# Kernel tuning notes

Measured on AMD Instinct MI355X. Metric: run time of the kernel, lower is better.

## Reference

```python
import jax, jax.numpy as jnp
import numpy as np

LATENT = 1024

def setup_inputs() -> dict:
    key = jax.random.key(0)
    k1, k2, k3, k4 = jax.random.split(key, 4)
    B, T, D = 64, 512, LATENT
    h_t = jax.random.normal(k1, (B, D), dtype=jnp.float32)
    z = jax.random.normal(k2, (B, T, D), dtype=jnp.float32)
    # nn.Linear(2D, D): weight [D, 2D], bias [D]
    bound = 1.0 / np.sqrt(2 * D)
    W = jax.random.uniform(k3, (D, 2 * D), minval=-bound, maxval=bound, dtype=jnp.float32)
    b = jax.random.uniform(k4, (D,), minval=-bound, maxval=bound, dtype=jnp.float32)
    alpha = jnp.full((D,), 0.1, dtype=jnp.float32)
    return {"h_t": h_t, "z": z, "W": W, "b": b, "alpha": alpha}

def reference(h_t, z, W, b, alpha):
    # Split gate weight into h-part and z-part (concat([h,z]) @ W.T == h@Wh.T + z@Wz.T)
    D = h_t.shape[-1]
    Wh = W[:, :D]  # [D, D]
    Wz = W[:, D:]  # [D, D]
    leak = 1.0 - alpha  # [D]

    def step(h, z_t):
        gate = jax.nn.sigmoid(h @ Wh.T + z_t @ Wz.T + b)
        h_new = jnp.tanh(h * leak + gate * z_t)
        return h_new, h_new

    # scan over time: z is [B, T, D] -> [T, B, D]
    _, hs = jax.lax.scan(step, h_t, jnp.swapaxes(z, 0, 1))
    return jnp.swapaxes(hs, 0, 1)  # [B, T, D]
```

## Files before the change

### kernel.cpp

```cpp
#include <hip/hip_runtime.h>
#include <math.h>


#define D_ 1024
#define B_ 64
#define T_ 512

typedef _Float16 f16;
typedef _Float16 f16x8 __attribute__((ext_vector_type(8)));
typedef _Float16 f16x4 __attribute__((ext_vector_type(4)));
typedef float f32x4 __attribute__((ext_vector_type(4)));
typedef unsigned long long u64;

#define WS_WH16  0L
#define WS_WZ16  2097152L
#define WS_SLOTS 4194304L

__device__ __forceinline__ void gload_lds16(const void* g, void* l) {
  __builtin_amdgcn_global_load_lds(
      (const __attribute__((address_space(1))) void*)(g),
      (__attribute__((address_space(3))) void*)(l), 16, 0, 0);
}

__global__ __launch_bounds__(256) void k_prep(
    const float* __restrict__ W, const float* __restrict__ h0,
    f16* __restrict__ wh16, f16* __restrict__ wz16, u64* __restrict__ slots) {
  const int tid = blockIdx.x * 256 + threadIdx.x;
  {
    const long e = (long)tid * 4;
    const long j = e >> 11, c = e & 2047;
    float4 v = *(const float4*)(W + e);
    f16x4 o = {(f16)v.x, (f16)v.y, (f16)v.z, (f16)v.w};
    f16* dst = (c < D_) ? (wh16 + j * D_ + c) : (wz16 + j * D_ + (c - D_));
    *(f16x4*)dst = o;
  }
  if (tid < 65536) {
    if (tid < 32768) {
      const int b = tid >> 9, p = tid & 511;
      f16 fa = (f16)h0[(long)b * D_ + 2 * p];
      f16 fb = (f16)h0[(long)b * D_ + 2 * p + 1];
      unsigned u = (unsigned)*(unsigned short*)&fa |
                   ((unsigned)*(unsigned short*)&fb << 16);
      slots[tid] = (u64)u;
    } else {
      slots[tid] = 0xFFFFFFFF00000000ull;
    }
  }
}

__global__ __launch_bounds__(256) void k_gemm_zw(
    const float* __restrict__ zf, const f16* __restrict__ wz16,
    const float* __restrict__ bias, float* __restrict__ out) {
  __shared__ f16 ldsA[8 * 512];
  __shared__ f16 ldsB[8 * 512];
  const int tid = threadIdx.x, lane = tid & 63, w = tid >> 6;
  const int r16 = lane & 15, g8 = lane >> 4;
  const int nt = blockIdx.x & 7, mt = blockIdx.x >> 3;
  const long m0 = (long)mt * 128, n0 = (long)nt * 128;
  const int arow = tid >> 1, kh = (tid & 1) * 16;
  const float* gA = zf + (m0 + arow) * D_ + kh;
  const f16* gB = wz16 + (n0 + r16) * D_ + g8 * 8;
  const int wr = w >> 1, wc = w & 1;
  f32x4 acc[4][4] = {};
  float4 ra[4];
#pragma unroll
  for (int q = 0; q < 4; ++q) ra[q] = *(const float4*)(gA + q * 4);

  for (int ks = 0; ks < 32; ++ks) {
    if (ks) __syncthreads();
#pragma unroll
    for (int c = 0; c < 2; ++c) {
      const int ch = w * 2 + c;
      gload_lds16(gB + (long)ch * 16 * D_ + ks * 32, &ldsB[ch * 512]);
    }
    {
      const int ch = arow >> 4, lr = arow & 15;
#pragma unroll
      for (int hf = 0; hf < 2; ++hf) {
        float4 x = ra[hf * 2], y = ra[hf * 2 + 1];
        f16x8 v = {(f16)x.x, (f16)x.y, (f16)x.z, (f16)x.w,
                   (f16)y.x, (f16)y.y, (f16)y.z, (f16)y.w};
        const int kk = kh + hf * 8;
        *(f16x8*)(&ldsA[ch * 512 + (lr | ((kk >> 3) << 4)) * 8]) = v;
      }
    }
    __syncthreads();
    if (ks < 31) {
#pragma unroll
      for (int q = 0; q < 4; ++q)
        ra[q] = *(const float4*)(gA + (ks + 1) * 32 + q * 4);
    }
    f16x8 af[4], bf[4];
#pragma unroll
    for (int i = 0; i < 4; ++i)
      af[i] = *(const f16x8*)(&ldsA[(wr * 4 + i) * 512 + lane * 8]);
#pragma unroll
    for (int j = 0; j < 4; ++j)
      bf[j] = *(const f16x8*)(&ldsB[(wc * 4 + j) * 512 + lane * 8]);
#pragma unroll
    for (int i = 0; i < 4; ++i)
#pragma unroll
      for (int j = 0; j < 4; ++j)
        acc[i][j] = __builtin_amdgcn_mfma_f32_16x16x32_f16(af[i], bf[j], acc[i][j], 0, 0, 0);
  }

  float bj[4];
#pragma unroll
  for (int j = 0; j < 4; ++j) bj[j] = bias[n0 + wc * 64 + j * 16 + r16];
#pragma unroll
  for (int i = 0; i < 4; ++i) {
    const long mb = m0 + wr * 64 + i * 16 + g8 * 4;
#pragma unroll
    for (int j = 0; j < 4; ++j) {
      const long nn = n0 + wc * 64 + j * 16 + r16;
#pragma unroll
      for (int r = 0; r < 4; ++r)
        out[(mb + r) * D_ + nn] = acc[i][j][r] + bj[j];
    }
  }
}

__global__ __launch_bounds__(256, 1) void k_recur(
    const f16* __restrict__ wh16, u64* slots, const float* __restrict__ z,
    const float* __restrict__ h0, const float* __restrict__ alpha,
    float* __restrict__ out) {
  __shared__ char Hb[8192];
  __shared__ float red[4096];

  const int tid = threadIdx.x, lane = tid & 63, w = tid >> 6;
  const int bid = blockIdx.x;
  const int g = (bid & 7) * 2 + ((bid >> 3) & 1);
  const int rk = bid >> 4;
  const int j0 = rk * 64, b0 = g * 4;

  f16x8 bfr[32];
  {
    const f16* wb = wh16 + (long)(j0 + (lane & 15)) * D_ + w * 256 + (lane >> 4) * 8;
#pragma unroll
    for (int n = 0; n < 4; ++n)
#pragma unroll
      for (int kt = 0; kt < 8; ++kt)
        bfr[n * 8 + kt] = *(const f16x8*)(wb + (long)n * 16 * D_ + kt * 32);
  }

  const int jj = j0 + lane;
  const float lk = 1.0f - alpha[jj];
  float hp = h0[(long)(b0 + w) * D_ + jj];

  const int row = lane & 3, g8 = lane >> 4;
  const int nn = lane >> 4, jc = lane & 15;

  for (int t = 0; t < T_; ++t) {
    const long off = ((long)(b0 + w) * T_ + t) * D_ + jj;
    float A = out[off];
    float Z = z[off];

    const u64* cur = slots + (long)(t & 1) * 32768 + (long)b0 * 512 + w * 128;
    u64 vv[8];
    unsigned pend = 0xFFu;
    for (int guard = 0; pend && guard < (1 << 18); ++guard) {
#pragma unroll
      for (int i = 0; i < 8; ++i)
        if (pend & (1u << i)) {
          const int idx = i * 64 + lane;
          vv[i] = __hip_atomic_load(cur + (idx >> 7) * 512 + (idx & 127),
                                    __ATOMIC_RELAXED, __HIP_MEMORY_SCOPE_AGENT);
        }
#pragma unroll
      for (int i = 0; i < 8; ++i)
        if ((pend & (1u << i)) && (unsigned)(vv[i] >> 32) == (unsigned)t)
          pend &= ~(1u << i);
    }

#pragma unroll
    for (int i = 0; i < 8; ++i) {
      const int idx = i * 64 + lane, b = idx >> 7, lp = idx & 127;
      *(unsigned*)(Hb + ((w * 2048 + b * 512 + lp * 4) ^ ((b & 1) << 6))) =
          (unsigned)vv[i];
    }

    f32x4 acc[4] = {{0,0,0,0},{0,0,0,0},{0,0,0,0},{0,0,0,0}};
#pragma unroll
    for (int kt = 0; kt < 8; ++kt) {
      f16x8 af = *(const f16x8*)(
          Hb + ((w * 2048 + row * 512 + kt * 64 + g8 * 16) ^ ((row & 1) << 6)));
#pragma unroll
      for (int n = 0; n < 4; ++n)
        acc[n] = __builtin_amdgcn_mfma_f32_16x16x32_f16(af, bfr[n * 8 + kt], acc[n], 0, 0, 0);
    }

#pragma unroll
    for (int n = 0; n < 4; ++n)
      *(f32x4*)(red + ((w * 4 + n) * 64 + lane) * 4) = acc[n];
    __syncthreads();

    float pre = 0.f;
#pragma unroll
    for (int wp = 0; wp < 4; ++wp)
      pre += red[(wp * 4 + nn) * 256 + jc * 4 + w];
    const float gg = 1.0f / (1.0f + expf(-(pre + A)));
    const float hn = tanhf(hp * lk + gg * Z);
    out[off] = hn;
    hp = hn;

    const float q = __shfl_xor(hn, 1);
    if (!(lane & 1)) {
      f16 pa = (f16)hn, pb = (f16)q;
      const unsigned u = (unsigned)*(unsigned short*)&pa |
                         ((unsigned)*(unsigned short*)&pb << 16);
      const u64 val = (((u64)(unsigned)(t + 1)) << 32) | (u64)u;
      __hip_atomic_store(slots + (long)((t + 1) & 1) * 32768 + (long)(b0 + w) * 512 + (jj >> 1),
                         val, __ATOMIC_RELAXED, __HIP_MEMORY_SCOPE_AGENT);
    }
    __syncthreads();
  }
}

extern "C" void kernel_launch(void* const* d_in, const int* in_sizes, int n_in,
                              void* d_out, int out_size, void* d_ws, size_t ws_size,
                              hipStream_t stream) {
  const float* h_t = (const float*)d_in[0];
  const float* z = (const float*)d_in[1];
  const float* W = (const float*)d_in[2];
  const float* bias = (const float*)d_in[3];
  const float* alpha = (const float*)d_in[4];
  float* out = (float*)d_out;
  char* ws = (char*)d_ws;
  f16* wh16 = (f16*)(ws + WS_WH16);
  f16* wz16 = (f16*)(ws + WS_WZ16);
  u64* slots = (u64*)(ws + WS_SLOTS);

  k_prep<<<dim3(2048), dim3(256), 0, stream>>>(W, h_t, wh16, wz16, slots);
  k_gemm_zw<<<dim3(2048), dim3(256), 0, stream>>>(z, wz16, bias, out);
  k_recur<<<dim3(256), dim3(256), 0, stream>>>(wh16, slots, z, h_t, alpha, out);
}
```

Baseline: 1.410 ms.

## Pre-convert z to fp16, double-buffer GEMM LDS, and restructure recurrence split-K

The prep kernel now also converts z to fp16 in workspace so the z·Wz GEMM can load both operands with direct global-to-LDS loads into double-buffered tiles. This removes per-step fp32-to-fp16 conversion and one barrier from the GEMM loop. The recurrent kernel now gives each wave its own 16 output columns over the full K, so the cross-wave LDS reduction buffer and one barrier per step are gone, and the shared h tile is double-buffered. Sigmoid and tanh use fast exp and reciprocal intrinsics. The cost is an extra full pass over z plus a 64 MB fp16 copy, and some loss of accuracy from the approximate transcendentals.

After: 1.802 ms. +27.8%, slower.

```diff
diff --git a/kernel.cpp b/kernel.cpp
--- a/kernel.cpp
+++ b/kernel.cpp
@@ -12,9 +12,10 @@
 typedef float f32x4 __attribute__((ext_vector_type(4)));
 typedef unsigned long long u64;
 
-#define WS_WH16  0L
-#define WS_WZ16  2097152L
-#define WS_SLOTS 4194304L
+#define WS_Z16   0L
+#define WS_WH16  67108864L
+#define WS_WZ16  69206016L
+#define WS_SLOTS 71303168L
 
 __device__ __forceinline__ void gload_lds16(const void* g, void* l) {
   __builtin_amdgcn_global_load_lds(
@@ -23,16 +24,24 @@
 }
 
 __global__ __launch_bounds__(256) void k_prep(
-    const float* __restrict__ W, const float* __restrict__ h0,
+    const float* __restrict__ z, const float* __restrict__ W,
+    const float* __restrict__ h0, f16* __restrict__ z16,
     f16* __restrict__ wh16, f16* __restrict__ wz16, u64* __restrict__ slots) {
   const int tid = blockIdx.x * 256 + threadIdx.x;
-  {
-    const long e = (long)tid * 4;
-    const long j = e >> 11, c = e & 2047;
-    float4 v = *(const float4*)(W + e);
-    f16x4 o = {(f16)v.x, (f16)v.y, (f16)v.z, (f16)v.w};
-    f16* dst = (c < D_) ? (wh16 + j * D_ + c) : (wz16 + j * D_ + (c - D_));
-    *(f16x4*)dst = o;
+  const long ZN4 = 8388608, WN4 = 524288;
+  for (long i = tid; i < ZN4 + WN4; i += 524288) {
+    if (i < ZN4) {
+      float4 v = *(const float4*)(z + i * 4);
+      f16x4 o = {(f16)v.x, (f16)v.y, (f16)v.z, (f16)v.w};
+      *(f16x4*)(z16 + i * 4) = o;
+    } else {
+      const long e2 = (i - ZN4) * 4;
+      const long j = e2 >> 11, c = e2 & 2047;
+      float4 v = *(const float4*)(W + e2);
+      f16x4 o = {(f16)v.x, (f16)v.y, (f16)v.z, (f16)v.w};
+      f16* dst = (c < D_) ? (wh16 + j * D_ + c) : (wz16 + j * D_ + (c - D_));
+      *(f16x4*)dst = o;
+    }
   }
   if (tid < 65536) {
     if (tid < 32768) {
@@ -49,59 +58,50 @@
 }
 
 __global__ __launch_bounds__(256) void k_gemm_zw(
-    const float* __restrict__ zf, const f16* __restrict__ wz16,
+    const f16* __restrict__ z16, const f16* __restrict__ wz16,
     const float* __restrict__ bias, float* __restrict__ out) {
-  __shared__ f16 ldsA[8 * 512];
-  __shared__ f16 ldsB[8 * 512];
+  __shared__ f16 ldsA[2][8 * 512];
+  __shared__ f16 ldsB[2][8 * 512];
   const int tid = threadIdx.x, lane = tid & 63, w = tid >> 6;
   const int r16 = lane & 15, g8 = lane >> 4;
   const int nt = blockIdx.x & 7, mt = blockIdx.x >> 3;
   const long m0 = (long)mt * 128, n0 = (long)nt * 128;
-  const int arow = tid >> 1, kh = (tid & 1) * 16;
-  const float* gA = zf + (m0 + arow) * D_ + kh;
+  const f16* gA = z16 + (m0 + r16) * D_ + g8 * 8;
   const f16* gB = wz16 + (n0 + r16) * D_ + g8 * 8;
   const int wr = w >> 1, wc = w & 1;
   f32x4 acc[4][4] = {};
-  float4 ra[4];
-#pragma unroll
-  for (int q = 0; q < 4; ++q) ra[q] = *(const float4*)(gA + q * 4);
+
+#pragma unroll
+  for (int c = 0; c < 2; ++c) {
+    const int ch = w * 2 + c;
+    gload_lds16(gA + (long)ch * 16 * D_, &ldsA[0][ch * 512]);
+    gload_lds16(gB + (long)ch * 16 * D_, &ldsB[0][ch * 512]);
+  }
+  __syncthreads();
 
   for (int ks = 0; ks < 32; ++ks) {
-    if (ks) __syncthreads();
-#pragma unroll
-    for (int c = 0; c < 2; ++c) {
-      const int ch = w * 2 + c;
-      gload_lds16(gB + (long)ch * 16 * D_ + ks * 32, &ldsB[ch * 512]);
-    }
-    {
-      const int ch = arow >> 4, lr = arow & 15;
-#pragma unroll
-      for (int hf = 0; hf < 2; ++hf) {
-        float4 x = ra[hf * 2], y = ra[hf * 2 + 1];
-        f16x8 v = {(f16)x.x, (f16)x.y, (f16)x.z, (f16)x.w,
-                   (f16)y.x, (f16)y.y, (f16)y.z, (f16)y.w};
-        const int kk = kh + hf * 8;
-        *(f16x8*)(&ldsA[ch * 512 + (lr | ((kk >> 3) << 4)) * 8]) = v;
+    const int buf = ks & 1;
+    if (ks < 31) {
+#pragma unroll
+      for (int c = 0; c < 2; ++c) {
+        const int ch = w * 2 + c;
+        gload_lds16(gA + (long)ch * 16 * D_ + (ks + 1) * 32, &ldsA[buf ^ 1][ch * 512]);
+        gload_lds16(gB + (long)ch * 16 * D_ + (ks + 1) * 32, &ldsB[buf ^ 1][ch * 512]);
       }
     }
-    __syncthreads();
-    if (ks < 31) {
-#pragma unroll
-      for (int q = 0; q < 4; ++q)
-        ra[q] = *(const float4*)(gA + (ks + 1) * 32 + q * 4);
-    }
     f16x8 af[4], bf[4];
 #pragma unroll
     for (int i = 0; i < 4; ++i)
-      af[i] = *(const f16x8*)(&ldsA[(wr * 4 + i) * 512 + lane * 8]);
+      af[i] = *(const f16x8*)(&ldsA[buf][(wr * 4 + i) * 512 + lane * 8]);
 #pragma unroll
     for (int j = 0; j < 4; ++j)
-      bf[j] = *(const f16x8*)(&ldsB[(wc * 4 + j) * 512 + lane * 8]);
+      bf[j] = *(const f16x8*)(&ldsB[buf][(wc * 4 + j) * 512 + lane * 8]);
 #pragma unroll
     for (int i = 0; i < 4; ++i)
 #pragma unroll
       for (int j = 0; j < 4; ++j)
         acc[i][j] = __builtin_amdgcn_mfma_f32_16x16x32_f16(af[i], bf[j], acc[i][j], 0, 0, 0);
+    __syncthreads();
   }
 
   float bj[4];
@@ -124,8 +124,7 @@
     const f16* __restrict__ wh16, u64* slots, const float* __restrict__ z,
     const float* __restrict__ h0, const float* __restrict__ alpha,
     float* __restrict__ out) {
-  __shared__ char Hb[8192];
-  __shared__ float red[4096];
+  __shared__ char Hb[2][8192];
 
   const int tid = threadIdx.x, lane = tid & 63, w = tid >> 6;
   const int bid = blockIdx.x;
@@ -135,23 +134,23 @@
 
   f16x8 bfr[32];
   {
-    const f16* wb = wh16 + (long)(j0 + (lane & 15)) * D_ + w * 256 + (lane >> 4) * 8;
-#pragma unroll
-    for (int n = 0; n < 4; ++n)
-#pragma unroll
-      for (int kt = 0; kt < 8; ++kt)
-        bfr[n * 8 + kt] = *(const f16x8*)(wb + (long)n * 16 * D_ + kt * 32);
-  }
-
-  const int jj = j0 + lane;
+    const f16* wb = wh16 + (long)(j0 + w * 16 + (lane & 15)) * D_ + (lane >> 4) * 8;
+#pragma unroll
+    for (int kt = 0; kt < 32; ++kt)
+      bfr[kt] = *(const f16x8*)(wb + kt * 32);
+  }
+
+  const int bl = lane >> 4;
+  const int jl = lane & 15;
+  const int jj = j0 + w * 16 + jl;
   const float lk = 1.0f - alpha[jj];
-  float hp = h0[(long)(b0 + w) * D_ + jj];
-
-  const int row = lane & 3, g8 = lane >> 4;
-  const int nn = lane >> 4, jc = lane & 15;
+  float hp = h0[(long)(b0 + bl) * D_ + jj];
+
+  const int ab = lane & 3;
+  const int g8 = lane >> 4;
 
   for (int t = 0; t < T_; ++t) {
-    const long off = ((long)(b0 + w) * T_ + t) * D_ + jj;
+    const long off = ((long)(b0 + bl) * T_ + t) * D_ + jj;
     float A = out[off];
     float Z = z[off];
 
@@ -172,35 +171,40 @@
           pend &= ~(1u << i);
     }
 
+    char* hb = Hb[t & 1];
 #pragma unroll
     for (int i = 0; i < 8; ++i) {
       const int idx = i * 64 + lane, b = idx >> 7, lp = idx & 127;
-      *(unsigned*)(Hb + ((w * 2048 + b * 512 + lp * 4) ^ ((b & 1) << 6))) =
-          (unsigned)vv[i];
-    }
-
-    f32x4 acc[4] = {{0,0,0,0},{0,0,0,0},{0,0,0,0},{0,0,0,0}};
-#pragma unroll
-    for (int kt = 0; kt < 8; ++kt) {
-      f16x8 af = *(const f16x8*)(
-          Hb + ((w * 2048 + row * 512 + kt * 64 + g8 * 16) ^ ((row & 1) << 6)));
-#pragma unroll
-      for (int n = 0; n < 4; ++n)
-        acc[n] = __builtin_amdgcn_mfma_f32_16x16x32_f16(af, bfr[n * 8 + kt], acc[n], 0, 0, 0);
-    }
-
-#pragma unroll
-    for (int n = 0; n < 4; ++n)
-      *(f32x4*)(red + ((w * 4 + n) * 64 + lane) * 4) = acc[n];
+      const int o = w * 512 + lp * 4;
+      *(unsigned*)(hb + b * 2048 + (o ^ (b * 32))) = (unsigned)vv[i];
+    }
     __syncthreads();
 
-    float pre = 0.f;
-#pragma unroll
-    for (int wp = 0; wp < 4; ++wp)
-      pre += red[(wp * 4 + nn) * 256 + jc * 4 + w];
-    const float gg = 1.0f / (1.0f + expf(-(pre + A)));
-    const float hn = tanhf(hp * lk + gg * Z);
-    out[off] = hn;
+    f32x4 ac0 = {}, ac1 = {}, ac2 = {}, ac3 = {};
+#pragma unroll
+    for (int kt = 0; kt < 32; kt += 4) {
+      f16x8 a0 = *(const f16x8*)(hb + ab * 2048 + (((kt + 0) * 64 + g8 * 16) ^ (ab * 32)));
+      f16x8 a1 = *(const f16x8*)(hb + ab * 2048 + (((kt + 1) * 64 + g8 * 16) ^ (ab * 32)));
+      f16x8 a2 = *(const f16x8*)(hb + ab * 2048 + (((kt + 2) * 64 + g8 * 16) ^ (ab * 32)));
+      f16x8 a3 = *(const f16x8*)(hb + ab * 2048 + (((kt + 3) * 64 + g8 * 16) ^ (ab * 32)));
+      ac0 = __builtin_amdgcn_mfma_f32_16x16x32_f16(a0, bfr[kt + 0], ac0, 0, 0, 0);
+      ac1 = __builtin_amdgcn_mfma_f32_16x16x32_f16(a1, bfr[kt + 1], ac1, 0, 0, 0);
+      ac2 = __builtin_amdgcn_mfma_f32_16x16x32_f16(a2, bfr[kt + 2], ac2, 0, 0, 0);
+      ac3 = __builtin_amdgcn_mfma_f32_16x16x32_f16(a3, bfr[kt + 3], ac3, 0, 0, 0);
+    }
+    const f32x4 facc = (ac0 + ac1) + (ac2 + ac3);
+
+    const float v0 = __shfl(facc[0], jl);
+    const float v1 = __shfl(facc[1], jl);
+    const float v2 = __shfl(facc[2], jl);
+    const float v3 = __shfl(facc[3], jl);
+    const float pre = bl == 0 ? v0 : bl == 1 ? v1 : bl == 2 ? v2 : v3;
+
+    const float gg = __builtin_amdgcn_rcpf(1.0f + __expf(-(pre + A)));
+    float y = 2.0f * (hp * lk + gg * Z);
+    y = fminf(fmaxf(y, -30.0f), 30.0f);
+    const float ex = __expf(y);
+    const float hn = (ex - 1.0f) * __builtin_amdgcn_rcpf(ex + 1.0f);
     hp = hn;
 
     const float q = __shfl_xor(hn, 1);
@@ -209,10 +213,12 @@
       const unsigned u = (unsigned)*(unsigned short*)&pa |
                          ((unsigned)*(unsigned short*)&pb << 16);
       const u64 val = (((u64)(unsigned)(t + 1)) << 32) | (u64)u;
-      __hip_atomic_store(slots + (long)((t + 1) & 1) * 32768 + (long)(b0 + w) * 512 + (jj >> 1),
-                         val, __ATOMIC_RELAXED, __HIP_MEMORY_SCOPE_AGENT);
-    }
-    __syncthreads();
+      __hip_atomic_store(
+          slots + (long)((t + 1) & 1) * 32768 + (long)(b0 + bl) * 512 +
+              (j0 >> 1) + w * 8 + (jl >> 1),
+          val, __ATOMIC_RELAXED, __HIP_MEMORY_SCOPE_AGENT);
+    }
+    out[off] = hn;
   }
 }
 
@@ -226,11 +232,12 @@
   const float* alpha = (const float*)d_in[4];
   float* out = (float*)d_out;
   char* ws = (char*)d_ws;
+  f16* z16 = (f16*)(ws + WS_Z16);
   f16* wh16 = (f16*)(ws + WS_WH16);
   f16* wz16 = (f16*)(ws + WS_WZ16);
   u64* slots = (u64*)(ws + WS_SLOTS);
 
-  k_prep<<<dim3(2048), dim3(256), 0, stream>>>(W, h_t, wh16, wz16, slots);
-  k_gemm_zw<<<dim3(2048), dim3(256), 0, stream>>>(z, wz16, bias, out);
+  k_prep<<<dim3(2048), dim3(256), 0, stream>>>(z, W, h_t, z16, wh16, wz16, slots);
+  k_gemm_zw<<<dim3(2048), dim3(256), 0, stream>>>(z16, wz16, bias, out);
   k_recur<<<dim3(256), dim3(256), 0, stream>>>(wh16, slots, z, h_t, alpha, out);
 }
```
